# Kernel optimization log

Measured on AMD Instinct MI355X. Metric: run time of the kernel, lower is better.

## Reference

```python
import jax, jax.numpy as jnp
import numpy as np

NUM_CP = 5      # num_control_points per edge
DEGREE = 3      # B-spline degree


def bspline_basis(x, n, d):
    """Cox-de Boor B-spline basis.
    x: [B, I] inputs; returns [B, I, n] basis values.
    Uniform knots on [-1, 1], length n + d + 1."""
    t = jnp.linspace(-1.0, 1.0, n + d + 1).astype(x.dtype)
    x_ = x[..., None]                       # [B, I, 1]
    # degree-0 indicator basis: [B, I, n+d]
    B = ((x_ >= t[:-1]) & (x_ < t[1:])).astype(x.dtype)
    for r in range(1, d + 1):
        m = n + d - r                       # number of basis funcs at this level
        left = (x_ - t[:m]) / (t[r:r + m] - t[:m]) * B[..., :m]
        right = (t[r + 1:r + 1 + m] - x_) / (t[r + 1:r + 1 + m] - t[1:1 + m]) * B[..., 1:m + 1]
        B = left + right
    return B                                # [B, I, n]


def setup_inputs() -> dict:
    key = jax.random.key(0)
    k1, k2, k3 = jax.random.split(key, 3)
    batch, input_dim, output_dim = 4096, 1024, 1024
    x = jax.random.uniform(k1, (batch, input_dim), dtype=jnp.float32)
    coeffs = jax.random.normal(k2, (input_dim, output_dim, NUM_CP), dtype=jnp.float32)
    importance = jax.random.normal(k3, (input_dim, output_dim), dtype=jnp.float32)
    return {"x": x, "coeffs": coeffs, "importance": importance}


def reference(x, coeffs, importance):
    # basis: [B, I, K]; per-edge spline weights scaled by importance: [I, O, K]
    basis = bspline_basis(x, NUM_CP, DEGREE)
    w = importance[..., None] * coeffs
    # out[b, o] = sum_{i,k} basis[b,i,k] * w[i,o,k]
    out = jnp.einsum('bik,iok->bo', basis, w)
    return out
```

## Files before the change

kernel.cpp:

```cpp
#include <hip/hip_runtime.h>
#include <stdint.h>

#define B_DIM 4096
#define I_DIM 1024
#define O_DIM 1024
#define KD    4096
#define OUT_N (B_DIM * O_DIM)

#define SPLITK 2
#define KCHUNK (KD / SPLITK)
#define NKT    (KCHUNK / 64)

typedef short v8s __attribute__((ext_vector_type(8)));
typedef float v4f __attribute__((ext_vector_type(4)));

__device__ __forceinline__ uint16_t f2bf(float f) {
    union { float f; uint32_t u; } v; v.f = f;
    uint32_t u = v.u;
    return (uint16_t)((u + 0x7FFFu + ((u >> 16) & 1u)) >> 16);
}
__device__ __forceinline__ float bf2f(uint32_t hi_bits) {
    union { uint32_t u; float f; } v; v.u = hi_bits; return v.f;
}

__device__ __forceinline__ void gload_lds16(const uint16_t* g, uint16_t* l) {
    __builtin_amdgcn_global_load_lds(
        (const __attribute__((address_space(1))) void*)g,
        (__attribute__((address_space(3))) void*)l,
        16, 0, 0);
}

__global__ void zero_kernel(float4* __restrict__ out, int n4) {
    int idx = blockIdx.x * blockDim.x + threadIdx.x;
    if (idx < n4) out[idx] = float4{0.f, 0.f, 0.f, 0.f};
}

__global__ void prep_kernel(const float* __restrict__ x,
                            const float* __restrict__ coeffs,
                            const float* __restrict__ imp,
                            uint16_t* __restrict__ A, uint16_t* __restrict__ WT) {
    __shared__ __align__(16) char lds[65536];
    int id = blockIdx.x;
    int t  = threadIdx.x;
    if (id < 512) {
        int b0 = id * 8;
#pragma unroll
        for (int bb = 0; bb < 8; ++bb) {
            int b = b0 + bb;
#pragma unroll
            for (int q = 0; q < 4; ++q) {
                int i = q * 256 + t;
                float xv = x[(size_t)b * I_DIM + i];
                float tt = 4.0f * xv;
                float fj = floorf(tt);
                fj = fminf(fmaxf(fj, 0.0f), 3.0f);
                int j4 = (int)fj;
                float u  = tt - fj;
                float um = 1.0f - u;
                float u2 = u * u, u3 = u2 * u;
                const float s = 1.0f / 6.0f;
                float w0 = um * um * um * s;
                float w1 = (3.0f * u3 - 6.0f * u2 + 4.0f) * s;
                float w2 = (-3.0f * u3 + 3.0f * u2 + 3.0f * u + 1.0f) * s;
                float w3 = u3 * s;
                float o0 = (j4 == 0) ? w0 : 0.0f;
                float o1 = (j4 == 0) ? w1 : (j4 == 1) ? w0 : 0.0f;
                float o2 = (j4 == 0) ? w2 : (j4 == 1) ? w1 : (j4 == 2) ? w0 : 0.0f;
                float o3 = (j4 == 0) ? w3 : (j4 == 1) ? w2 : (j4 == 2) ? w1 : w0;
                union { uint16_t h[4]; uint2 v; } pk;
                pk.h[0] = f2bf(o0); pk.h[1] = f2bf(o1);
                pk.h[2] = f2bf(o2); pk.h[3] = f2bf(o3);
                *(uint2*)(A + (size_t)b * KD + (size_t)i * 4) = pk.v;
            }
        }
    } else {
        int bid = id - 512;
        int i0 = (bid & 31) * 32;
        int o0 = (bid >> 5) * 256;
        int o  = o0 + t;
        const int swz = (t & 7) << 4;
        union { uint16_t h[8]; uint4 v; } pk;
#pragma unroll
        for (int ii = 0; ii < 32; ++ii) {
            int i = i0 + ii;
            float im = imp[(size_t)i * O_DIM + o];
            const float* cp = coeffs + ((size_t)i * O_DIM + o) * 5;
            int base = (ii & 1) * 4;
            pk.h[base + 0] = f2bf(im * cp[1]);
            pk.h[base + 1] = f2bf(im * cp[2]);
            pk.h[base + 2] = f2bf(im * cp[3]);
            pk.h[base + 3] = f2bf(im * cp[4]);
            if (ii & 1)
                *(uint4*)(lds + t * 256 + (((ii - 1) * 8) ^ swz)) = pk.v;
        }
        __syncthreads();
#pragma unroll
        for (int j = 0; j < 16; ++j) {
            int c   = t + 256 * j;
            int row = c >> 4;
            int u   = c & 15;
            uint4 v = *(const uint4*)(lds + row * 256 + ((u * 16) ^ ((row & 7) << 4)));
            *(uint4*)(WT + (size_t)(o0 + row) * KD + i0 * 4 + u * 8) = v;
        }
    }
}


template<int PARTIAL>
__global__ __launch_bounds__(512, 4)
void gemm_kernel(const uint16_t* __restrict__ A, const uint16_t* __restrict__ WT,
                 float* __restrict__ out, uint16_t* __restrict__ P) {
    int hw  = blockIdx.x;
    int lid = (hw & 7) * 64 + (hw >> 3);
    int nt = lid & 7, sk = (lid >> 3) & 1, mt = lid >> 4;

    int t    = threadIdx.x;
    int lane = t & 63;
    int wid  = t >> 6;
    int wr = wid >> 2, wc = wid & 3;

    __shared__ __align__(16) uint16_t smem[32768];
    uint16_t* sA0 = smem;
    uint16_t* sB0 = smem + 16384;

    const uint16_t* Ab = A  + (size_t)(mt * 128) * KD + sk * KCHUNK;
    const uint16_t* Bb = WT + (size_t)(nt * 128) * KD + sk * KCHUNK;

    const int r0  = t >> 3;
    const int kel = ((((t & 7) << 4) ^ ((r0 & 7) << 4)) >> 1);

    auto stage = [&](int buf, int kt) {
        const uint16_t* ga = Ab + (size_t)r0 * KD + kt * 64 + kel;
        const uint16_t* gb = Bb + (size_t)r0 * KD + kt * 64 + kel;
        gload_lds16(ga,                   sA0 + buf * 8192 + t * 8);
        gload_lds16(ga + (size_t)64 * KD, sA0 + buf * 8192 + 4096 + t * 8);
        gload_lds16(gb,                   sB0 + buf * 8192 + t * 8);
        gload_lds16(gb + (size_t)64 * KD, sB0 + buf * 8192 + 4096 + t * 8);
    };

    v8s af[4][2], bf[2][2];
    v4f acc[4][2] = {};

    const int swz = (lane & 7) << 4;
    const int kb0 = (lane >> 4) << 4;
    const int lra = wr * 64 + (lane & 15);
    const int lrb = wc * 32 + (lane & 15);

    stage(0, 0);
    asm volatile("s_waitcnt vmcnt(0)" ::: "memory");
    __builtin_amdgcn_s_barrier();

#pragma unroll 2
    for (int g = 0; g < NKT; ++g) {
        const int buf = g & 1;
        if (g + 1 < NKT) stage(buf ^ 1, g + 1);

        const char* ba = (const char*)(sA0 + buf * 8192);
        const char* bb = (const char*)(sB0 + buf * 8192);
#pragma unroll
        for (int mb = 0; mb < 4; ++mb)
#pragma unroll
            for (int ks = 0; ks < 2; ++ks)
                af[mb][ks] = *(const v8s*)(ba + (size_t)(lra + mb * 16) * 128 + ((kb0 + ks * 64) ^ swz));
#pragma unroll
        for (int nb = 0; nb < 2; ++nb)
#pragma unroll
            for (int ks = 0; ks < 2; ++ks)
                bf[nb][ks] = *(const v8s*)(bb + (size_t)(lrb + nb * 16) * 128 + ((kb0 + ks * 64) ^ swz));

        asm volatile("s_waitcnt lgkmcnt(0)" ::: "memory");
        __builtin_amdgcn_s_setprio(1);
#pragma unroll
        for (int mb = 0; mb < 4; ++mb)
#pragma unroll
            for (int nb = 0; nb < 2; ++nb)
#pragma unroll
                for (int ks = 0; ks < 2; ++ks)
                    acc[mb][nb] = __builtin_amdgcn_mfma_f32_16x16x32_bf16(af[mb][ks], bf[nb][ks],
                                                                          acc[mb][nb], 0, 0, 0);
        __builtin_amdgcn_s_setprio(0);

        if (g + 1 < NKT) asm volatile("s_waitcnt vmcnt(0)" ::: "memory");
        __builtin_amdgcn_s_barrier();
    }

    const int oc  = lane & 15;
    const int orr = (lane >> 4) * 4;
    if (PARTIAL) {
        uint16_t* wlds = smem + wid * 2048;
#pragma unroll
        for (int mb = 0; mb < 4; ++mb)
#pragma unroll
            for (int nb = 0; nb < 2; ++nb)
#pragma unroll
                for (int r = 0; r < 4; ++r) {
                    int row = mb * 16 + orr + r;
                    int col = nb * 16 + oc;
                    wlds[row * 32 + (col ^ (((row >> 2) & 3) << 3))] = f2bf(acc[mb][nb][r]);
                }
        asm volatile("s_waitcnt lgkmcnt(0)" ::: "memory");
        uint16_t* pb = P + (size_t)sk * OUT_N
                         + (size_t)(mt * 128 + wr * 64) * O_DIM + nt * 128 + wc * 32;
#pragma unroll
        for (int j = 0; j < 4; ++j) {
            int c   = j * 64 + lane;
            int row = c >> 2;
            int u   = (c & 3) * 8;
            uint4 v = *(const uint4*)&wlds[row * 32 + (u ^ (((row >> 2) & 3) << 3))];
            *(uint4*)(pb + (size_t)row * O_DIM + u) = v;
        }
    } else {
        float* ob = out + (size_t)(mt * 128 + wr * 64) * O_DIM + nt * 128 + wc * 32;
#pragma unroll
        for (int mb = 0; mb < 4; ++mb)
#pragma unroll
            for (int nb = 0; nb < 2; ++nb)
#pragma unroll
                for (int r = 0; r < 4; ++r)
                    atomicAdd(&ob[(size_t)(mb * 16 + orr + r) * O_DIM + nb * 16 + oc],
                              acc[mb][nb][r]);
    }
}

__global__ void reduce_kernel(const uint16_t* __restrict__ P, float* __restrict__ out) {
    size_t idx = ((size_t)blockIdx.x * 256 + threadIdx.x) * 8;
    float s[8] = {0, 0, 0, 0, 0, 0, 0, 0};
#pragma unroll
    for (int sk = 0; sk < SPLITK; ++sk) {
        uint4 v = *(const uint4*)(P + (size_t)sk * OUT_N + idx);
        uint32_t w[4] = {v.x, v.y, v.z, v.w};
#pragma unroll
        for (int j = 0; j < 4; ++j) {
            s[2 * j]     += bf2f((w[j] & 0xFFFFu) << 16);
            s[2 * j + 1] += bf2f(w[j] & 0xFFFF0000u);
        }
    }
    float4 lo = {s[0], s[1], s[2], s[3]};
    float4 hi = {s[4], s[5], s[6], s[7]};
    *(float4*)(out + idx)     = lo;
    *(float4*)(out + idx + 4) = hi;
}

extern "C" void kernel_launch(void* const* d_in, const int* in_sizes, int n_in,
                              void* d_out, int out_size, void* d_ws, size_t ws_size,
                              hipStream_t stream) {
    const float* x      = (const float*)d_in[0];
    const float* coeffs = (const float*)d_in[1];
    const float* imp    = (const float*)d_in[2];
    float* out = (float*)d_out;

    const size_t A_ELEMS  = (size_t)B_DIM * KD;
    const size_t WT_ELEMS = (size_t)O_DIM * KD;
    const size_t P_ELEMS  = (size_t)SPLITK * OUT_N;
    uint16_t* A  = (uint16_t*)d_ws;
    uint16_t* WT = A + A_ELEMS;
    uint16_t* P  = WT + WT_ELEMS;
    const size_t need = (A_ELEMS + WT_ELEMS + P_ELEMS) * 2;

    hipLaunchKernelGGL(prep_kernel, dim3(512 + 128), dim3(256), 0, stream,
                       x, coeffs, imp, A, WT);
    if (ws_size >= need) {
        hipLaunchKernelGGL((gemm_kernel<1>), dim3(512), dim3(512), 0, stream, A, WT, out, P);
        hipLaunchKernelGGL(reduce_kernel, dim3(OUT_N / 8 / 256), dim3(256), 0, stream, P, out);
    } else {
        hipLaunchKernelGGL(zero_kernel, dim3((OUT_N / 4) / 256), dim3(256), 0, stream,
                           (float4*)out, OUT_N / 4);
        hipLaunchKernelGGL((gemm_kernel<0>), dim3(512), dim3(512), 0, stream, A, WT, out, P);
    }
}
```

Baseline: 61.28 us.

## Fuse B-spline basis evaluation into GEMM A-tile staging

The basis matrix A is no longer built by the prep kernel and written to global memory. Each GEMM block now loads raw x values, evaluates the cubic basis in registers and writes the bf16 tile straight into LDS, overlapping this with the MFMA loop. This removes a 32 MB write plus repeated reads of A. In exchange, basis math is recomputed once per N-tile (8x redundancy), and the VALU work and LDS stores inside the main loop may compete with the MFMAs.

```diff
diff --git a/kernel.cpp b/kernel.cpp
--- a/kernel.cpp
+++ b/kernel.cpp
@@ -30,85 +30,70 @@
         16, 0, 0);
 }
 
+__device__ __forceinline__ void eval_basis4(float xv, uint16_t* h) {
+    float tt = 4.0f * xv;
+    float fj = floorf(tt);
+    fj = fminf(fmaxf(fj, 0.0f), 3.0f);
+    int j4 = (int)fj;
+    float u  = tt - fj;
+    float um = 1.0f - u;
+    float u2 = u * u, u3 = u2 * u;
+    const float s = 1.0f / 6.0f;
+    float w0 = um * um * um * s;
+    float w1 = (3.0f * u3 - 6.0f * u2 + 4.0f) * s;
+    float w2 = (-3.0f * u3 + 3.0f * u2 + 3.0f * u + 1.0f) * s;
+    float w3 = u3 * s;
+    float o0 = (j4 == 0) ? w0 : 0.0f;
+    float o1 = (j4 == 0) ? w1 : (j4 == 1) ? w0 : 0.0f;
+    float o2 = (j4 == 0) ? w2 : (j4 == 1) ? w1 : (j4 == 2) ? w0 : 0.0f;
+    float o3 = (j4 == 0) ? w3 : (j4 == 1) ? w2 : (j4 == 2) ? w1 : w0;
+    h[0] = f2bf(o0); h[1] = f2bf(o1); h[2] = f2bf(o2); h[3] = f2bf(o3);
+}
+
 __global__ void zero_kernel(float4* __restrict__ out, int n4) {
     int idx = blockIdx.x * blockDim.x + threadIdx.x;
     if (idx < n4) out[idx] = float4{0.f, 0.f, 0.f, 0.f};
 }
 
-__global__ void prep_kernel(const float* __restrict__ x,
-                            const float* __restrict__ coeffs,
+__global__ void prep_kernel(const float* __restrict__ coeffs,
                             const float* __restrict__ imp,
-                            uint16_t* __restrict__ A, uint16_t* __restrict__ WT) {
+                            uint16_t* __restrict__ WT) {
     __shared__ __align__(16) char lds[65536];
-    int id = blockIdx.x;
-    int t  = threadIdx.x;
-    if (id < 512) {
-        int b0 = id * 8;
-#pragma unroll
-        for (int bb = 0; bb < 8; ++bb) {
-            int b = b0 + bb;
-#pragma unroll
-            for (int q = 0; q < 4; ++q) {
-                int i = q * 256 + t;
-                float xv = x[(size_t)b * I_DIM + i];
-                float tt = 4.0f * xv;
-                float fj = floorf(tt);
-                fj = fminf(fmaxf(fj, 0.0f), 3.0f);
-                int j4 = (int)fj;
-                float u  = tt - fj;
-                float um = 1.0f - u;
-                float u2 = u * u, u3 = u2 * u;
-                const float s = 1.0f / 6.0f;
-                float w0 = um * um * um * s;
-                float w1 = (3.0f * u3 - 6.0f * u2 + 4.0f) * s;
-                float w2 = (-3.0f * u3 + 3.0f * u2 + 3.0f * u + 1.0f) * s;
-                float w3 = u3 * s;
-                float o0 = (j4 == 0) ? w0 : 0.0f;
-                float o1 = (j4 == 0) ? w1 : (j4 == 1) ? w0 : 0.0f;
-                float o2 = (j4 == 0) ? w2 : (j4 == 1) ? w1 : (j4 == 2) ? w0 : 0.0f;
-                float o3 = (j4 == 0) ? w3 : (j4 == 1) ? w2 : (j4 == 2) ? w1 : w0;
-                union { uint16_t h[4]; uint2 v; } pk;
-                pk.h[0] = f2bf(o0); pk.h[1] = f2bf(o1);
-                pk.h[2] = f2bf(o2); pk.h[3] = f2bf(o3);
-                *(uint2*)(A + (size_t)b * KD + (size_t)i * 4) = pk.v;
-            }
-        }
-    } else {
-        int bid = id - 512;
-        int i0 = (bid & 31) * 32;
-        int o0 = (bid >> 5) * 256;
-        int o  = o0 + t;
-        const int swz = (t & 7) << 4;
-        union { uint16_t h[8]; uint4 v; } pk;
-#pragma unroll
-        for (int ii = 0; ii < 32; ++ii) {
-            int i = i0 + ii;
-            float im = imp[(size_t)i * O_DIM + o];
-            const float* cp = coeffs + ((size_t)i * O_DIM + o) * 5;
-            int base = (ii & 1) * 4;
-            pk.h[base + 0] = f2bf(im * cp[1]);
-            pk.h[base + 1] = f2bf(im * cp[2]);
-            pk.h[base + 2] = f2bf(im * cp[3]);
-            pk.h[base + 3] = f2bf(im * cp[4]);
-            if (ii & 1)
-                *(uint4*)(lds + t * 256 + (((ii - 1) * 8) ^ swz)) = pk.v;
-        }
-        __syncthreads();
-#pragma unroll
-        for (int j = 0; j < 16; ++j) {
-            int c   = t + 256 * j;
-            int row = c >> 4;
-            int u   = c & 15;
-            uint4 v = *(const uint4*)(lds + row * 256 + ((u * 16) ^ ((row & 7) << 4)));
-            *(uint4*)(WT + (size_t)(o0 + row) * KD + i0 * 4 + u * 8) = v;
-        }
+    int bid = blockIdx.x;
+    int t   = threadIdx.x;
+    int i0 = (bid & 31) * 32;
+    int o0 = (bid >> 5) * 256;
+    int o  = o0 + t;
+    const int swz = (t & 7) << 4;
+    union { uint16_t h[8]; uint4 v; } pk;
+#pragma unroll
+    for (int ii = 0; ii < 32; ++ii) {
+        int i = i0 + ii;
+        float im = imp[(size_t)i * O_DIM + o];
+        const float* cp = coeffs + ((size_t)i * O_DIM + o) * 5;
+        int base = (ii & 1) * 4;
+        pk.h[base + 0] = f2bf(im * cp[1]);
+        pk.h[base + 1] = f2bf(im * cp[2]);
+        pk.h[base + 2] = f2bf(im * cp[3]);
+        pk.h[base + 3] = f2bf(im * cp[4]);
+        if (ii & 1)
+            *(uint4*)(lds + t * 256 + (((ii - 1) * 8) ^ swz)) = pk.v;
+    }
+    __syncthreads();
+#pragma unroll
+    for (int j = 0; j < 16; ++j) {
+        int c   = t + 256 * j;
+        int row = c >> 4;
+        int u   = c & 15;
+        uint4 v = *(const uint4*)(lds + row * 256 + ((u * 16) ^ ((row & 7) << 4)));
+        *(uint4*)(WT + (size_t)(o0 + row) * KD + i0 * 4 + u * 8) = v;
     }
 }
 
 
 template<int PARTIAL>
 __global__ __launch_bounds__(512, 4)
-void gemm_kernel(const uint16_t* __restrict__ A, const uint16_t* __restrict__ WT,
+void gemm_kernel(const float* __restrict__ x, const uint16_t* __restrict__ WT,
                  float* __restrict__ out, uint16_t* __restrict__ P) {
     int hw  = blockIdx.x;
     int lid = (hw & 7) * 64 + (hw >> 3);
@@ -123,19 +108,30 @@
     uint16_t* sA0 = smem;
     uint16_t* sB0 = smem + 16384;
 
-    const uint16_t* Ab = A  + (size_t)(mt * 128) * KD + sk * KCHUNK;
     const uint16_t* Bb = WT + (size_t)(nt * 128) * KD + sk * KCHUNK;
 
-    const int r0  = t >> 3;
-    const int kel = ((((t & 7) << 4) ^ ((r0 & 7) << 4)) >> 1);
-
-    auto stage = [&](int buf, int kt) {
-        const uint16_t* ga = Ab + (size_t)r0 * KD + kt * 64 + kel;
-        const uint16_t* gb = Bb + (size_t)r0 * KD + kt * 64 + kel;
-        gload_lds16(ga,                   sA0 + buf * 8192 + t * 8);
-        gload_lds16(ga + (size_t)64 * KD, sA0 + buf * 8192 + 4096 + t * 8);
+    const int r0b = t >> 3;
+    const int kel = ((((t & 7) << 4) ^ ((r0b & 7) << 4)) >> 1);
+    auto stageB = [&](int buf, int kt) {
+        const uint16_t* gb = Bb + (size_t)r0b * KD + kt * 64 + kel;
         gload_lds16(gb,                   sB0 + buf * 8192 + t * 8);
         gload_lds16(gb + (size_t)64 * KD, sB0 + buf * 8192 + 4096 + t * 8);
+    };
+
+    const int ra  = t >> 2;
+    const int swA = (ra & 7) << 4;
+    const float* xb = x + (size_t)(mt * 128 + ra) * I_DIM + sk * 512 + 4 * (t & 3);
+    uint16_t* aw = sA0 + ra * 64;
+    const int off0 = ((2 * (t & 3) * 16) ^ swA) >> 1;
+    const int off1 = (((2 * (t & 3) + 1) * 16) ^ swA) >> 1;
+
+    auto stageA = [&](int buf, float4 xq) {
+        union { uint16_t h[8]; uint4 v; } c0, c1;
+        eval_basis4(xq.x, c0.h); eval_basis4(xq.y, c0.h + 4);
+        eval_basis4(xq.z, c1.h); eval_basis4(xq.w, c1.h + 4);
+        uint16_t* b = aw + buf * 8192;
+        *(uint4*)(b + off0) = c0.v;
+        *(uint4*)(b + off1) = c1.v;
     };
 
     v8s af[4][2], bf[2][2];
@@ -146,14 +142,22 @@
     const int lra = wr * 64 + (lane & 15);
     const int lrb = wc * 32 + (lane & 15);
 
-    stage(0, 0);
-    asm volatile("s_waitcnt vmcnt(0)" ::: "memory");
+    {
+        float4 xq = *(const float4*)(xb);
+        stageB(0, 0);
+        stageA(0, xq);
+    }
+    asm volatile("s_waitcnt vmcnt(0) lgkmcnt(0)" ::: "memory");
     __builtin_amdgcn_s_barrier();
 
 #pragma unroll 2
     for (int g = 0; g < NKT; ++g) {
         const int buf = g & 1;
-        if (g + 1 < NKT) stage(buf ^ 1, g + 1);
+        float4 xq;
+        if (g + 1 < NKT) {
+            xq = *(const float4*)(xb + (g + 1) * 16);
+            stageB(buf ^ 1, g + 1);
+        }
 
         const char* ba = (const char*)(sA0 + buf * 8192);
         const char* bb = (const char*)(sB0 + buf * 8192);
@@ -180,7 +184,9 @@
                                                                           acc[mb][nb], 0, 0, 0);
         __builtin_amdgcn_s_setprio(0);
 
-        if (g + 1 < NKT) asm volatile("s_waitcnt vmcnt(0)" ::: "memory");
+        if (g + 1 < NKT) stageA(buf ^ 1, xq);
+
+        asm volatile("s_waitcnt vmcnt(0) lgkmcnt(0)" ::: "memory");
         __builtin_amdgcn_s_barrier();
     }
 
@@ -249,22 +255,19 @@
     const float* imp    = (const float*)d_in[2];
     float* out = (float*)d_out;
 
-    const size_t A_ELEMS  = (size_t)B_DIM * KD;
     const size_t WT_ELEMS = (size_t)O_DIM * KD;
     const size_t P_ELEMS  = (size_t)SPLITK * OUT_N;
-    uint16_t* A  = (uint16_t*)d_ws;
-    uint16_t* WT = A + A_ELEMS;
+    uint16_t* WT = (uint16_t*)d_ws;
     uint16_t* P  = WT + WT_ELEMS;
-    const size_t need = (A_ELEMS + WT_ELEMS + P_ELEMS) * 2;
-
-    hipLaunchKernelGGL(prep_kernel, dim3(512 + 128), dim3(256), 0, stream,
-                       x, coeffs, imp, A, WT);
+    const size_t need = (WT_ELEMS + P_ELEMS) * 2;
+
+    hipLaunchKernelGGL(prep_kernel, dim3(128), dim3(256), 0, stream, coeffs, imp, WT);
     if (ws_size >= need) {
-        hipLaunchKernelGGL((gemm_kernel<1>), dim3(512), dim3(512), 0, stream, A, WT, out, P);
+        hipLaunchKernelGGL((gemm_kernel<1>), dim3(512), dim3(512), 0, stream, x, WT, out, P);
         hipLaunchKernelGGL(reduce_kernel, dim3(OUT_N / 8 / 256), dim3(256), 0, stream, P, out);
     } else {
         hipLaunchKernelGGL(zero_kernel, dim3((OUT_N / 4) / 256), dim3(256), 0, stream,
                            (float4*)out, OUT_N / 4);
-        hipLaunchKernelGGL((gemm_kernel<0>), dim3(512), dim3(512), 0, stream, A, WT, out, P);
-    }
-}
+        hipLaunchKernelGGL((gemm_kernel<0>), dim3(512), dim3(512), 0, stream, x, WT, out, P);
+    }
+}
```

Measured after the change: 80.75 us. 31.8% more time.

## Split K-tile into two half-phases with triple-buffered B prefetch

Applied to the files above, without the earlier changes.

Restructures the GEMM main loop into two half-K phases per tile, each loading half the fragments then issuing MFMAs. A is double-buffered and B is triple-buffered two tiles ahead, with the A and B global loads interleaved between the phases. It waits with vmcnt(2) instead of draining all loads, so more memory transfers stay in flight during compute. The cost is more LDS (40960 shorts) and extra barriers, which may lower occupancy and add sync overhead.

```diff
diff --git a/kernel.cpp b/kernel.cpp
--- a/kernel.cpp
+++ b/kernel.cpp
@@ -119,7 +119,7 @@
     int wid  = t >> 6;
     int wr = wid >> 2, wc = wid & 3;
 
-    __shared__ __align__(16) uint16_t smem[32768];
+    __shared__ __align__(16) uint16_t smem[40960];
     uint16_t* sA0 = smem;
     uint16_t* sB0 = smem + 16384;
 
@@ -129,16 +129,18 @@
     const int r0  = t >> 3;
     const int kel = ((((t & 7) << 4) ^ ((r0 & 7) << 4)) >> 1);
 
-    auto stage = [&](int buf, int kt) {
+    auto stageA = [&](int buf, int kt) {
         const uint16_t* ga = Ab + (size_t)r0 * KD + kt * 64 + kel;
-        const uint16_t* gb = Bb + (size_t)r0 * KD + kt * 64 + kel;
         gload_lds16(ga,                   sA0 + buf * 8192 + t * 8);
         gload_lds16(ga + (size_t)64 * KD, sA0 + buf * 8192 + 4096 + t * 8);
+    };
+    auto stageB = [&](int buf, int kt) {
+        const uint16_t* gb = Bb + (size_t)r0 * KD + kt * 64 + kel;
         gload_lds16(gb,                   sB0 + buf * 8192 + t * 8);
         gload_lds16(gb + (size_t)64 * KD, sB0 + buf * 8192 + 4096 + t * 8);
     };
 
-    v8s af[4][2], bf[2][2];
+    v8s af[4], bf[2];
     v4f acc[4][2] = {};
 
     const int swz = (lane & 7) << 4;
@@ -146,42 +148,61 @@
     const int lra = wr * 64 + (lane & 15);
     const int lrb = wc * 32 + (lane & 15);
 
-    stage(0, 0);
-    asm volatile("s_waitcnt vmcnt(0)" ::: "memory");
+    stageB(0, 0);
+    stageA(0, 0);
+    stageB(1, 1);
+    asm volatile("s_waitcnt vmcnt(2)" ::: "memory");
     __builtin_amdgcn_s_barrier();
 
-#pragma unroll 2
+    int bBr = 0;
     for (int g = 0; g < NKT; ++g) {
-        const int buf = g & 1;
-        if (g + 1 < NKT) stage(buf ^ 1, g + 1);
-
-        const char* ba = (const char*)(sA0 + buf * 8192);
-        const char* bb = (const char*)(sB0 + buf * 8192);
-#pragma unroll
-        for (int mb = 0; mb < 4; ++mb)
-#pragma unroll
-            for (int ks = 0; ks < 2; ++ks)
-                af[mb][ks] = *(const v8s*)(ba + (size_t)(lra + mb * 16) * 128 + ((kb0 + ks * 64) ^ swz));
+        const int bufA = g & 1;
+        const char* ba = (const char*)(sA0 + bufA * 8192);
+        const char* bb = (const char*)(sB0 + bBr * 8192);
+        const int bBs = bBr >= 1 ? bBr - 1 : 2;
+
+#pragma unroll
+        for (int mb = 0; mb < 4; ++mb)
+            af[mb] = *(const v8s*)(ba + (size_t)(lra + mb * 16) * 128 + (kb0 ^ swz));
 #pragma unroll
         for (int nb = 0; nb < 2; ++nb)
-#pragma unroll
-            for (int ks = 0; ks < 2; ++ks)
-                bf[nb][ks] = *(const v8s*)(bb + (size_t)(lrb + nb * 16) * 128 + ((kb0 + ks * 64) ^ swz));
-
+            bf[nb] = *(const v8s*)(bb + (size_t)(lrb + nb * 16) * 128 + (kb0 ^ swz));
+        if (g + 1 < NKT) stageA(bufA ^ 1, g + 1);
+        __builtin_amdgcn_s_barrier();
         asm volatile("s_waitcnt lgkmcnt(0)" ::: "memory");
         __builtin_amdgcn_s_setprio(1);
 #pragma unroll
         for (int mb = 0; mb < 4; ++mb)
 #pragma unroll
             for (int nb = 0; nb < 2; ++nb)
-#pragma unroll
-                for (int ks = 0; ks < 2; ++ks)
-                    acc[mb][nb] = __builtin_amdgcn_mfma_f32_16x16x32_bf16(af[mb][ks], bf[nb][ks],
-                                                                          acc[mb][nb], 0, 0, 0);
+                acc[mb][nb] = __builtin_amdgcn_mfma_f32_16x16x32_bf16(af[mb], bf[nb],
+                                                                      acc[mb][nb], 0, 0, 0);
         __builtin_amdgcn_s_setprio(0);
-
-        if (g + 1 < NKT) asm volatile("s_waitcnt vmcnt(0)" ::: "memory");
-        __builtin_amdgcn_s_barrier();
+        __builtin_amdgcn_s_barrier();
+
+#pragma unroll
+        for (int mb = 0; mb < 4; ++mb)
+            af[mb] = *(const v8s*)(ba + (size_t)(lra + mb * 16) * 128 + ((kb0 + 64) ^ swz));
+#pragma unroll
+        for (int nb = 0; nb < 2; ++nb)
+            bf[nb] = *(const v8s*)(bb + (size_t)(lrb + nb * 16) * 128 + ((kb0 + 64) ^ swz));
+        if (g + 2 < NKT) stageB(bBs, g + 2);
+        __builtin_amdgcn_s_barrier();
+        asm volatile("s_waitcnt lgkmcnt(0)" ::: "memory");
+        __builtin_amdgcn_s_setprio(1);
+#pragma unroll
+        for (int mb = 0; mb < 4; ++mb)
+#pragma unroll
+            for (int nb = 0; nb < 2; ++nb)
+                acc[mb][nb] = __builtin_amdgcn_mfma_f32_16x16x32_bf16(af[mb], bf[nb],
+                                                                      acc[mb][nb], 0, 0, 0);
+        __builtin_amdgcn_s_setprio(0);
+
+        if (g < NKT - 2)       asm volatile("s_waitcnt vmcnt(2)" ::: "memory");
+        else if (g == NKT - 2) asm volatile("s_waitcnt vmcnt(0)" ::: "memory");
+        __builtin_amdgcn_s_barrier();
+
+        bBr = bBr == 2 ? 0 : bBr + 1;
     }
 
     const int oc  = lane & 15;
```

New measurement: 62.95 us. 2.7% more time.
